# Kernel tuning notes

Measured on AMD Instinct MI355X. Metric: run time of the kernel, lower is better.

The kernel has to match this reference:

```python
import jax, jax.numpy as jnp
import numpy as np

E = 1024   # d_model
H = 16     # nhead
DH = E // H
F = 4096   # dim_feedforward
B, S = 4, 1024
EPS = 1e-5


def setup_inputs() -> dict:
    key = jax.random.key(0)
    ks = jax.random.split(key, 12)
    s = 0.02
    return {
        "src": jax.random.normal(ks[0], (B, S, E), jnp.float32),
        "src_mask": jnp.zeros((S, S), jnp.float32),
        "w_qkv": jax.random.normal(ks[1], (3 * E, E), jnp.float32) * s,
        "b_qkv": jnp.zeros((3 * E,), jnp.float32),
        "w_o": jax.random.normal(ks[2], (E, E), jnp.float32) * s,
        "b_o": jnp.zeros((E,), jnp.float32),
        "w1": jax.random.normal(ks[3], (F, E), jnp.float32) * s,
        "b1": jnp.zeros((F,), jnp.float32),
        "w2": jax.random.normal(ks[4], (E, F), jnp.float32) * s,
        "b2": jnp.zeros((E,), jnp.float32),
        "ln1_g": jnp.ones((E,), jnp.float32),
        "ln1_b": jnp.zeros((E,), jnp.float32),
        "ln2_g": jnp.ones((E,), jnp.float32),
        "ln2_b": jnp.zeros((E,), jnp.float32),
    }


def _layer_norm(x, g, b):
    mu = jnp.mean(x, axis=-1, keepdims=True)
    var = jnp.mean(jnp.square(x - mu), axis=-1, keepdims=True)
    return (x - mu) * jax.lax.rsqrt(var + EPS) * g + b


def reference(src, src_mask, w_qkv, b_qkv, w_o, b_o, w1, b1, w2, b2,
              ln1_g, ln1_b, ln2_g, ln2_b):
    # dropout in eval mode (identity). Math matches nn.MultiheadAttention
    # with need_weights=True, average_attn_weights=False.
    b, s, e = src.shape
    qkv = src @ w_qkv.T + b_qkv                      # [B,S,3E]
    q, k, v = jnp.split(qkv, 3, axis=-1)
    q = q.reshape(b, s, H, DH)
    k = k.reshape(b, s, H, DH)
    v = v.reshape(b, s, H, DH)
    scale = 1.0 / np.sqrt(DH)
    scores = jnp.einsum('bqhd,bkhd->bhqk', q, k) * scale + src_mask  # [B,H,S,S]
    attn_weights = jax.nn.softmax(scores, axis=-1)                   # [B,H,S,S]
    ctx = jnp.einsum('bhqk,bkhd->bqhd', attn_weights, v).reshape(b, s, e)
    attn_out = ctx @ w_o.T + b_o
    x = _layer_norm(src + attn_out, ln1_g, ln1_b)
    ffn = jax.nn.relu(x @ w1.T + b1) @ w2.T + b2
    x = _layer_norm(x + ffn, ln2_g, ln2_b)
    return x, attn_weights
```

## Files before the change

kernel.cpp:

```cpp
#include <hip/hip_runtime.h>
#include <cstdint>

typedef __bf16 bf16;
typedef bf16 bf16x8 __attribute__((ext_vector_type(8)));
typedef bf16 bf16x4 __attribute__((ext_vector_type(4)));
typedef float f32x4 __attribute__((ext_vector_type(4)));
typedef uint32_t u32;

static constexpr int E_ = 1024;
static constexpr int H_ = 16;
static constexpr int DH_ = 64;
static constexpr int F_ = 4096;
static constexpr int B_ = 4;
static constexpr int S_ = 1024;
static constexpr long TOK = (long)B_ * S_;

__device__ static __forceinline__ void gld16(const void* g, void* l) {
  __builtin_amdgcn_global_load_lds(
      (const __attribute__((address_space(1))) u32*)g,
      (__attribute__((address_space(3))) u32*)l, 16, 0, 0);
}

__device__ __forceinline__ f32x4 mfma16(bf16x8 a, bf16x8 b, f32x4 c) {
  return __builtin_amdgcn_mfma_f32_16x16x32_bf16(a, b, c, 0, 0, 0);
}

__global__ __launch_bounds__(256) void f2b_kernel(const float* __restrict__ in,
                                                  bf16* __restrict__ out, int n8) {
  int v = blockIdx.x * 256 + threadIdx.x;
  if (v >= n8) return;
  const float4* p = (const float4*)in + (long)v * 2;
  float4 a = p[0], b = p[1];
  bf16x8 o = {(bf16)a.x, (bf16)a.y, (bf16)a.z, (bf16)a.w,
              (bf16)b.x, (bf16)b.y, (bf16)b.z, (bf16)b.w};
  *((bf16x8*)out + v) = o;
}

enum { EPI_BIAS_F32 = 0, EPI_BIAS_RELU_BF16 = 1, EPI_QKV = 2, EPI_BIAS_RES_F32 = 3 };

template <int EPI>
__global__ __launch_bounds__(256, 2) void gemm_nt(
    const bf16* __restrict__ A, const bf16* __restrict__ Bm,
    float* __restrict__ Cf, bf16* __restrict__ Cb,
    bf16* __restrict__ Qh, bf16* __restrict__ Kh, bf16* __restrict__ Vt,
    const float* __restrict__ bias, const float* __restrict__ res,
    int K, int ldc) {
  __shared__ bf16 As[128 * 64];
  __shared__ bf16 Bs[128 * 64];
  const int tid = threadIdx.x, lane = tid & 63, wave = tid >> 6;
  const int quad = lane >> 4, l16 = lane & 15;
  const int wm = wave >> 1, wn = wave & 1;
  const int row0 = blockIdx.y * 128, col0 = blockIdx.x * 128;

  const long ldab = (long)K * 2;
  const char* Ag = (const char*)A +
                   (long)(row0 + wave * 32 + (lane >> 3)) * ldab + (lane & 7) * 16;
  const char* Bg = (const char*)Bm +
                   (long)(col0 + wave * 32 + (lane >> 3)) * ldab + (lane & 7) * 16;
  char* Al = (char*)As + wave * 4096 + lane * 16;
  char* Bl = (char*)Bs + wave * 4096 + lane * 16;

  f32x4 acc[4][4];
#pragma unroll
  for (int i = 0; i < 4; i++)
#pragma unroll
    for (int j = 0; j < 4; j++) acc[i][j] = (f32x4){0.f, 0.f, 0.f, 0.f};

  for (int k0 = 0; k0 < K; k0 += 64) {
    __syncthreads();
#pragma unroll
    for (int c = 0; c < 4; c++) gld16(Ag + (long)c * 8 * ldab + k0 * 2, Al + c * 1024);
#pragma unroll
    for (int c = 0; c < 4; c++) gld16(Bg + (long)c * 8 * ldab + k0 * 2, Bl + c * 1024);
    __syncthreads();
#pragma unroll
    for (int kk = 0; kk < 2; kk++) {
      bf16x8 af[4], bfr[4];
#pragma unroll
      for (int i = 0; i < 4; i++)
        af[i] = *(const bf16x8*)&As[(wm * 64 + i * 16 + l16) * 64 + kk * 32 + quad * 8];
#pragma unroll
      for (int j = 0; j < 4; j++)
        bfr[j] = *(const bf16x8*)&Bs[(wn * 64 + j * 16 + l16) * 64 + kk * 32 + quad * 8];
#pragma unroll
      for (int i = 0; i < 4; i++)
#pragma unroll
        for (int j = 0; j < 4; j++) acc[i][j] = mfma16(af[i], bfr[j], acc[i][j]);
    }
  }

#pragma unroll
  for (int i = 0; i < 4; i++)
#pragma unroll
    for (int j = 0; j < 4; j++)
#pragma unroll
      for (int r = 0; r < 4; r++) {
        int row = row0 + wm * 64 + i * 16 + quad * 4 + r;
        int col = col0 + wn * 64 + j * 16 + l16;
        float v = acc[i][j][r];
        if constexpr (EPI == EPI_BIAS_F32) {
          Cf[(long)row * ldc + col] = v + bias[col];
        } else if constexpr (EPI == EPI_BIAS_RES_F32) {
          Cf[(long)row * ldc + col] = v + bias[col] + res[(long)row * ldc + col];
        } else if constexpr (EPI == EPI_BIAS_RELU_BF16) {
          Cb[(long)row * ldc + col] = (bf16)fmaxf(v + bias[col], 0.f);
        } else {
          float t = v + bias[col];
          int b_ = row >> 10, s_ = row & 1023;
          int which = col >> 10, nn = col & 1023;
          int h_ = nn >> 6, d_ = nn & 63;
          if (which == 2) {
            Vt[(((long)(b_ * H_ + h_)) * DH_ + d_) * S_ + s_] = (bf16)t;
          } else {
            long q = (((long)(b_ * H_ + h_)) * S_ + s_) * DH_ + d_;
            if (which == 0) Qh[q] = (bf16)t;
            else Kh[q] = (bf16)t;
          }
        }
      }
}

__global__ __launch_bounds__(256, 2) void attn_pass1(
    const bf16* __restrict__ Q, const bf16* __restrict__ K,
    const float* __restrict__ mask, float* __restrict__ rowsum) {
  __shared__ bf16 Qs[128 * 64];
  __shared__ bf16 Ks[128 * 64];
  const int tid = threadIdx.x, lane = tid & 63, wave = tid >> 6;
  const int quad = lane >> 4, l16 = lane & 15;
  const int q0 = blockIdx.x * 128, bh = blockIdx.y;
  const bf16* Qb = Q + ((long)bh * S_ + q0) * DH_;
  const bf16* Kb = K + (long)bh * S_ * DH_;

  {
    const char* g = (const char*)Qb + wave * 4096 + lane * 16;
    char* l = (char*)Qs + wave * 4096 + lane * 16;
#pragma unroll
    for (int c = 0; c < 4; c++) gld16(g + c * 1024, l + c * 1024);
  }

  float rs[2][4];
#pragma unroll
  for (int i = 0; i < 2; i++)
#pragma unroll
    for (int r = 0; r < 4; r++) rs[i][r] = 0.f;

  for (int t = 0; t < 8; t++) {
    __syncthreads();
    {
      const char* g = (const char*)Kb + (long)t * 16384 + wave * 4096 + lane * 16;
      char* l = (char*)Ks + wave * 4096 + lane * 16;
#pragma unroll
      for (int c = 0; c < 4; c++) gld16(g + c * 1024, l + c * 1024);
    }
    __syncthreads();
    f32x4 acc[2][8];
#pragma unroll
    for (int i = 0; i < 2; i++)
#pragma unroll
      for (int j = 0; j < 8; j++) acc[i][j] = (f32x4){0.f, 0.f, 0.f, 0.f};
#pragma unroll
    for (int kk = 0; kk < 2; kk++) {
      bf16x8 af[2], bfr[8];
#pragma unroll
      for (int i = 0; i < 2; i++)
        af[i] = *(const bf16x8*)&Qs[(wave * 32 + i * 16 + l16) * 64 + kk * 32 + quad * 8];
#pragma unroll
      for (int j = 0; j < 8; j++)
        bfr[j] = *(const bf16x8*)&Ks[(j * 16 + l16) * 64 + kk * 32 + quad * 8];
#pragma unroll
      for (int i = 0; i < 2; i++)
#pragma unroll
        for (int j = 0; j < 8; j++) acc[i][j] = mfma16(af[i], bfr[j], acc[i][j]);
    }
#pragma unroll
    for (int i = 0; i < 2; i++)
#pragma unroll
      for (int j = 0; j < 8; j++)
#pragma unroll
        for (int r = 0; r < 4; r++) {
          int qr = q0 + wave * 32 + i * 16 + quad * 4 + r;
          int gcol = t * 128 + j * 16 + l16;
          float sv = acc[i][j][r] * 0.125f + mask[(long)qr * S_ + gcol];
          rs[i][r] += __expf(sv);
        }
  }
#pragma unroll
  for (int i = 0; i < 2; i++)
#pragma unroll
    for (int r = 0; r < 4; r++) {
      float v = rs[i][r];
      v += __shfl_xor(v, 1);
      v += __shfl_xor(v, 2);
      v += __shfl_xor(v, 4);
      v += __shfl_xor(v, 8);
      if (l16 == 0)
        rowsum[(long)bh * S_ + q0 + wave * 32 + i * 16 + quad * 4 + r] = v;
    }
}

__global__ __launch_bounds__(256, 2) void attn_pass2(
    const bf16* __restrict__ Q, const bf16* __restrict__ K,
    const bf16* __restrict__ V, const float* __restrict__ mask,
    const float* __restrict__ rowsum, float* __restrict__ W,
    bf16* __restrict__ ctxb) {
  __shared__ bf16 Qs[128 * 64];
  __shared__ bf16 Ks[128 * 64];
  __shared__ bf16 Ps[128 * 136];
  const int tid = threadIdx.x, lane = tid & 63, wave = tid >> 6;
  const int quad = lane >> 4, l16 = lane & 15;
  const int q0 = blockIdx.x * 128, bh = blockIdx.y;
  const bf16* Qb = Q + ((long)bh * S_ + q0) * DH_;
  const bf16* Kb = K + (long)bh * S_ * DH_;
  const bf16* Vb = V + (long)bh * DH_ * S_;

  float rinv[2][4];
#pragma unroll
  for (int i = 0; i < 2; i++)
#pragma unroll
    for (int r = 0; r < 4; r++)
      rinv[i][r] =
          1.0f / rowsum[(long)bh * S_ + q0 + wave * 32 + i * 16 + quad * 4 + r];

  {
    const char* g = (const char*)Qb + wave * 4096 + lane * 16;
    char* l = (char*)Qs + wave * 4096 + lane * 16;
#pragma unroll
    for (int c = 0; c < 4; c++) gld16(g + c * 1024, l + c * 1024);
  }

  f32x4 cacc[2][4];
#pragma unroll
  for (int i = 0; i < 2; i++)
#pragma unroll
    for (int j = 0; j < 4; j++) cacc[i][j] = (f32x4){0.f, 0.f, 0.f, 0.f};

  for (int t = 0; t < 8; t++) {
    __syncthreads();
    {
      const char* g = (const char*)Kb + (long)t * 16384 + wave * 4096 + lane * 16;
      char* l = (char*)Ks + wave * 4096 + lane * 16;
#pragma unroll
      for (int c = 0; c < 4; c++) gld16(g + c * 1024, l + c * 1024);
    }
    __syncthreads();
    f32x4 acc[2][8];
#pragma unroll
    for (int i = 0; i < 2; i++)
#pragma unroll
      for (int j = 0; j < 8; j++) acc[i][j] = (f32x4){0.f, 0.f, 0.f, 0.f};
#pragma unroll
    for (int kk = 0; kk < 2; kk++) {
      bf16x8 af[2], bfr[8];
#pragma unroll
      for (int i = 0; i < 2; i++)
        af[i] = *(const bf16x8*)&Qs[(wave * 32 + i * 16 + l16) * 64 + kk * 32 + quad * 8];
#pragma unroll
      for (int j = 0; j < 8; j++)
        bfr[j] = *(const bf16x8*)&Ks[(j * 16 + l16) * 64 + kk * 32 + quad * 8];
#pragma unroll
      for (int i = 0; i < 2; i++)
#pragma unroll
        for (int j = 0; j < 8; j++) acc[i][j] = mfma16(af[i], bfr[j], acc[i][j]);
    }
#pragma unroll
    for (int i = 0; i < 2; i++)
#pragma unroll
      for (int j = 0; j < 8; j++)
#pragma unroll
        for (int r = 0; r < 4; r++) {
          int ql = wave * 32 + i * 16 + quad * 4 + r;
          int qr = q0 + ql;
          int col = j * 16 + l16, gcol = t * 128 + col;
          float u = __expf(acc[i][j][r] * 0.125f + mask[(long)qr * S_ + gcol]) *
                    rinv[i][r];
          __builtin_nontemporal_store(u, &W[((long)bh * S_ + qr) * S_ + gcol]);
          Ps[ql * 136 + col] = (bf16)u;
        }
    __syncthreads();
#pragma unroll
    for (int kk = 0; kk < 4; kk++) {
      bf16x8 pf[2], vf[4];
#pragma unroll
      for (int i = 0; i < 2; i++)
        pf[i] = *(const bf16x8*)&Ps[(wave * 32 + i * 16 + l16) * 136 + kk * 32 + quad * 8];
#pragma unroll
      for (int j = 0; j < 4; j++)
        vf[j] = *(const bf16x8*)(Vb + (long)(j * 16 + l16) * S_ + t * 128 +
                                 kk * 32 + quad * 8);
#pragma unroll
      for (int i = 0; i < 2; i++)
#pragma unroll
        for (int j = 0; j < 4; j++) cacc[i][j] = mfma16(pf[i], vf[j], cacc[i][j]);
    }
  }
  const int b_ = bh >> 4, h_ = bh & 15;
#pragma unroll
  for (int i = 0; i < 2; i++)
#pragma unroll
    for (int j = 0; j < 4; j++)
#pragma unroll
      for (int r = 0; r < 4; r++) {
        int qr = q0 + wave * 32 + i * 16 + quad * 4 + r;
        ctxb[((long)b_ * S_ + qr) * E_ + h_ * 64 + j * 16 + l16] =
            (bf16)cacc[i][j][r];
      }
}

__global__ __launch_bounds__(256) void ln_kernel(
    const float* __restrict__ a, const float* __restrict__ g,
    const float* __restrict__ beta, float* __restrict__ outf,
    bf16* __restrict__ outb) {
  const int tid = threadIdx.x;
  const int wave = tid >> 6, lane = tid & 63;
  long base = (long)blockIdx.x * E_ + tid * 4;
  float4 x = *(const float4*)(a + base);
  float s = x.x + x.y + x.z + x.w;
  float sq = x.x * x.x + x.y * x.y + x.z * x.z + x.w * x.w;
#pragma unroll
  for (int o = 32; o; o >>= 1) { s += __shfl_xor(s, o); sq += __shfl_xor(sq, o); }
  __shared__ float rs[4], rq[4];
  if (!lane) { rs[wave] = s; rq[wave] = sq; }
  __syncthreads();
  s = rs[0] + rs[1] + rs[2] + rs[3];
  sq = rq[0] + rq[1] + rq[2] + rq[3];
  float mu = s * (1.f / E_);
  float var = sq * (1.f / E_) - mu * mu;
  float rstd = rsqrtf(var + 1e-5f);
  int c = tid * 4;
  float4 gg = *(const float4*)(g + c);
  float4 bb = *(const float4*)(beta + c);
  float o0 = (x.x - mu) * rstd * gg.x + bb.x;
  float o1 = (x.y - mu) * rstd * gg.y + bb.y;
  float o2 = (x.z - mu) * rstd * gg.z + bb.z;
  float o3 = (x.w - mu) * rstd * gg.w + bb.w;
  if (outf) *(float4*)(outf + base) = make_float4(o0, o1, o2, o3);
  if (outb) {
    bf16x4 ob = {(bf16)o0, (bf16)o1, (bf16)o2, (bf16)o3};
    *(bf16x4*)(outb + base) = ob;
  }
}

extern "C" void kernel_launch(void* const* d_in, const int* in_sizes, int n_in,
                              void* d_out, int out_size, void* d_ws, size_t ws_size,
                              hipStream_t stream) {
  const float* src   = (const float*)d_in[0];
  const float* mask  = (const float*)d_in[1];
  const float* w_qkv = (const float*)d_in[2];
  const float* b_qkv = (const float*)d_in[3];
  const float* w_o   = (const float*)d_in[4];
  const float* b_o   = (const float*)d_in[5];
  const float* w1    = (const float*)d_in[6];
  const float* b1    = (const float*)d_in[7];
  const float* w2    = (const float*)d_in[8];
  const float* b2    = (const float*)d_in[9];
  const float* ln1g  = (const float*)d_in[10];
  const float* ln1b  = (const float*)d_in[11];
  const float* ln2g  = (const float*)d_in[12];
  const float* ln2b  = (const float*)d_in[13];

  float* out = (float*)d_out;
  float* attnW = out + TOK * E_;

  char* w = (char*)d_ws;
  auto alloc = [&](size_t bytes) {
    void* p = w;
    w += (bytes + 255) & ~(size_t)255;
    return p;
  };
  bf16* srcb  = (bf16*)alloc(TOK * E_ * 2);
  bf16* wqkvb = (bf16*)alloc((size_t)3 * E_ * E_ * 2);
  bf16* wob   = (bf16*)alloc((size_t)E_ * E_ * 2);
  bf16* w1b   = (bf16*)alloc((size_t)F_ * E_ * 2);
  bf16* w2b   = (bf16*)alloc((size_t)E_ * F_ * 2);
  bf16* Qh    = (bf16*)alloc((size_t)B_ * H_ * S_ * DH_ * 2);
  bf16* Kh    = (bf16*)alloc((size_t)B_ * H_ * S_ * DH_ * 2);
  bf16* Vt    = (bf16*)alloc((size_t)B_ * H_ * DH_ * S_ * 2);
  bf16* ctxb  = (bf16*)alloc(TOK * E_ * 2);
  float* attn_out = (float*)alloc(TOK * E_ * 4);
  float* x1f  = (float*)alloc(TOK * E_ * 4);
  bf16* x1b   = (bf16*)alloc(TOK * E_ * 2);
  bf16* h1b   = (bf16*)alloc(TOK * (size_t)F_ * 2);
  float* ffn2 = (float*)alloc(TOK * E_ * 4);
  float* rowsum = (float*)alloc((size_t)B_ * H_ * S_ * 4);

  auto f2b = [&](const float* in, bf16* o, long n) {
    int n8 = (int)(n / 8);
    f2b_kernel<<<(n8 + 255) / 256, 256, 0, stream>>>(in, o, n8);
  };
  f2b(src, srcb, TOK * E_);
  f2b(w_qkv, wqkvb, (long)3 * E_ * E_);
  f2b(w_o, wob, (long)E_ * E_);
  f2b(w1, w1b, (long)F_ * E_);
  f2b(w2, w2b, (long)E_ * F_);

  gemm_nt<EPI_QKV><<<dim3(3 * E_ / 128, TOK / 128), 256, 0, stream>>>(
      srcb, wqkvb, nullptr, nullptr, Qh, Kh, Vt, b_qkv, nullptr, E_, 0);

  attn_pass1<<<dim3(S_ / 128, B_ * H_), 256, 0, stream>>>(Qh, Kh, mask, rowsum);
  attn_pass2<<<dim3(S_ / 128, B_ * H_), 256, 0, stream>>>(Qh, Kh, Vt, mask,
                                                          rowsum, attnW, ctxb);

  gemm_nt<EPI_BIAS_RES_F32><<<dim3(E_ / 128, TOK / 128), 256, 0, stream>>>(
      ctxb, wob, attn_out, nullptr, nullptr, nullptr, nullptr, b_o, src, E_, E_);

  ln_kernel<<<TOK, 256, 0, stream>>>(attn_out, ln1g, ln1b, x1f, x1b);

  gemm_nt<EPI_BIAS_RELU_BF16><<<dim3(F_ / 128, TOK / 128), 256, 0, stream>>>(
      x1b, w1b, nullptr, h1b, nullptr, nullptr, nullptr, b1, nullptr, E_, F_);

  gemm_nt<EPI_BIAS_RES_F32><<<dim3(E_ / 128, TOK / 128), 256, 0, stream>>>(
      h1b, w2b, ffn2, nullptr, nullptr, nullptr, nullptr, b2, x1f, F_, E_);

  ln_kernel<<<TOK, 256, 0, stream>>>(ffn2, ln2g, ln2b, out, nullptr);
}
```

Before: 648.5 us.

## Merge fp32-to-bf16 casts, add BN-templated GEMM, transpose V through LDS

Five separate fp32-to-bf16 conversion launches become one kernel that dispatches on flat index ranges. The GEMM gets a BN template parameter, and the two N=1024 GEMMs use 64-wide tiles so more blocks fill the GPU. The QKV epilogue now stages V tiles through a swizzled LDS transpose so it can write V^T with 16-byte vector stores instead of strided scalar stores. The smaller tiles lower per-block data reuse and add more blocks, and the merged cast kernel hardcodes the buffer offsets.

```diff
diff --git a/kernel.cpp b/kernel.cpp
--- a/kernel.cpp
+++ b/kernel.cpp
@@ -25,99 +25,148 @@
   return __builtin_amdgcn_mfma_f32_16x16x32_bf16(a, b, c, 0, 0, 0);
 }
 
-__global__ __launch_bounds__(256) void f2b_kernel(const float* __restrict__ in,
-                                                  bf16* __restrict__ out, int n8) {
-  int v = blockIdx.x * 256 + threadIdx.x;
-  if (v >= n8) return;
-  const float4* p = (const float4*)in + (long)v * 2;
+__global__ __launch_bounds__(256) void f2b_all(
+    const float* __restrict__ s0, bf16* __restrict__ d0,
+    const float* __restrict__ s1, bf16* __restrict__ d1,
+    const float* __restrict__ s2, bf16* __restrict__ d2,
+    const float* __restrict__ s3, bf16* __restrict__ d3,
+    const float* __restrict__ s4, bf16* __restrict__ d4) {
+  long v = (long)blockIdx.x * 256 + threadIdx.x;
+  const float* in;
+  bf16* out;
+  long off;
+  if (v < 524288)        { in = s0; out = d0; off = v; }
+  else if (v < 917504)   { in = s1; out = d1; off = v - 524288; }
+  else if (v < 1048576)  { in = s2; out = d2; off = v - 917504; }
+  else if (v < 1572864)  { in = s3; out = d3; off = v - 1048576; }
+  else                   { in = s4; out = d4; off = v - 1572864; }
+  const float4* p = (const float4*)in + off * 2;
   float4 a = p[0], b = p[1];
   bf16x8 o = {(bf16)a.x, (bf16)a.y, (bf16)a.z, (bf16)a.w,
               (bf16)b.x, (bf16)b.y, (bf16)b.z, (bf16)b.w};
-  *((bf16x8*)out + v) = o;
+  *((bf16x8*)out + off) = o;
 }
 
 enum { EPI_BIAS_F32 = 0, EPI_BIAS_RELU_BF16 = 1, EPI_QKV = 2, EPI_BIAS_RES_F32 = 3 };
 
-template <int EPI>
+template <int EPI, int BN>
 __global__ __launch_bounds__(256, 2) void gemm_nt(
     const bf16* __restrict__ A, const bf16* __restrict__ Bm,
     float* __restrict__ Cf, bf16* __restrict__ Cb,
     bf16* __restrict__ Qh, bf16* __restrict__ Kh, bf16* __restrict__ Vt,
     const float* __restrict__ bias, const float* __restrict__ res,
     int K, int ldc) {
-  __shared__ bf16 As[128 * 64];
-  __shared__ bf16 Bs[128 * 64];
+  constexpr int NJ = BN / 32;
+  __shared__ bf16 Sm[128 * 64 + BN * 64];
+  bf16* As = Sm;
+  bf16* Bs = Sm + 128 * 64;
   const int tid = threadIdx.x, lane = tid & 63, wave = tid >> 6;
   const int quad = lane >> 4, l16 = lane & 15;
   const int wm = wave >> 1, wn = wave & 1;
-  const int row0 = blockIdx.y * 128, col0 = blockIdx.x * 128;
+  const int row0 = blockIdx.y * 128, col0 = blockIdx.x * BN;
 
   const long ldab = (long)K * 2;
   const char* Ag = (const char*)A +
                    (long)(row0 + wave * 32 + (lane >> 3)) * ldab + (lane & 7) * 16;
   const char* Bg = (const char*)Bm +
-                   (long)(col0 + wave * 32 + (lane >> 3)) * ldab + (lane & 7) * 16;
-  char* Al = (char*)As + wave * 4096 + lane * 16;
-  char* Bl = (char*)Bs + wave * 4096 + lane * 16;
-
-  f32x4 acc[4][4];
+                   (long)(col0 + wave * (BN / 4) + (lane >> 3)) * ldab + (lane & 7) * 16;
+  char* Al = (char*)As + (wave * 32 + (lane >> 3)) * 128 + (lane & 7) * 16;
+  char* Bl = (char*)Bs + (wave * (BN / 4) + (lane >> 3)) * 128 + (lane & 7) * 16;
+
+  f32x4 acc[4][NJ];
 #pragma unroll
   for (int i = 0; i < 4; i++)
 #pragma unroll
-    for (int j = 0; j < 4; j++) acc[i][j] = (f32x4){0.f, 0.f, 0.f, 0.f};
+    for (int j = 0; j < NJ; j++) acc[i][j] = (f32x4){0.f, 0.f, 0.f, 0.f};
 
   for (int k0 = 0; k0 < K; k0 += 64) {
     __syncthreads();
 #pragma unroll
     for (int c = 0; c < 4; c++) gld16(Ag + (long)c * 8 * ldab + k0 * 2, Al + c * 1024);
 #pragma unroll
-    for (int c = 0; c < 4; c++) gld16(Bg + (long)c * 8 * ldab + k0 * 2, Bl + c * 1024);
+    for (int c = 0; c < BN / 32; c++) gld16(Bg + (long)c * 8 * ldab + k0 * 2, Bl + c * 1024);
     __syncthreads();
 #pragma unroll
     for (int kk = 0; kk < 2; kk++) {
-      bf16x8 af[4], bfr[4];
+      bf16x8 af[4], bfr[NJ];
 #pragma unroll
       for (int i = 0; i < 4; i++)
         af[i] = *(const bf16x8*)&As[(wm * 64 + i * 16 + l16) * 64 + kk * 32 + quad * 8];
 #pragma unroll
-      for (int j = 0; j < 4; j++)
-        bfr[j] = *(const bf16x8*)&Bs[(wn * 64 + j * 16 + l16) * 64 + kk * 32 + quad * 8];
+      for (int j = 0; j < NJ; j++)
+        bfr[j] = *(const bf16x8*)&Bs[(wn * (BN / 2) + j * 16 + l16) * 64 + kk * 32 + quad * 8];
 #pragma unroll
       for (int i = 0; i < 4; i++)
 #pragma unroll
-        for (int j = 0; j < 4; j++) acc[i][j] = mfma16(af[i], bfr[j], acc[i][j]);
-    }
-  }
-
-#pragma unroll
-  for (int i = 0; i < 4; i++)
-#pragma unroll
-    for (int j = 0; j < 4; j++)
-#pragma unroll
-      for (int r = 0; r < 4; r++) {
-        int row = row0 + wm * 64 + i * 16 + quad * 4 + r;
-        int col = col0 + wn * 64 + j * 16 + l16;
-        float v = acc[i][j][r];
-        if constexpr (EPI == EPI_BIAS_F32) {
-          Cf[(long)row * ldc + col] = v + bias[col];
-        } else if constexpr (EPI == EPI_BIAS_RES_F32) {
-          Cf[(long)row * ldc + col] = v + bias[col] + res[(long)row * ldc + col];
-        } else if constexpr (EPI == EPI_BIAS_RELU_BF16) {
-          Cb[(long)row * ldc + col] = (bf16)fmaxf(v + bias[col], 0.f);
-        } else {
-          float t = v + bias[col];
-          int b_ = row >> 10, s_ = row & 1023;
-          int which = col >> 10, nn = col & 1023;
-          int h_ = nn >> 6, d_ = nn & 63;
-          if (which == 2) {
-            Vt[(((long)(b_ * H_ + h_)) * DH_ + d_) * S_ + s_] = (bf16)t;
-          } else {
+        for (int j = 0; j < NJ; j++) acc[i][j] = mfma16(af[i], bfr[j], acc[i][j]);
+    }
+  }
+
+  if constexpr (EPI == EPI_QKV) {
+    const int which = col0 >> 10;
+    if (which == 2) {
+      bf16* T = Sm;
+      __syncthreads();
+#pragma unroll
+      for (int i = 0; i < 4; i++)
+#pragma unroll
+        for (int j = 0; j < NJ; j++)
+#pragma unroll
+          for (int r = 0; r < 4; r++) {
+            int row_l = wm * 64 + i * 16 + quad * 4 + r;
+            int col_l = wn * 64 + j * 16 + l16;
+            float t = acc[i][j][r] + bias[col0 + col_l];
+            T[col_l * 128 + (row_l ^ ((col_l & 7) << 4))] = (bf16)t;
+          }
+      __syncthreads();
+      const int b_ = row0 >> 10;
+      const int s0 = row0 & 1023;
+#pragma unroll
+      for (int g = 0; g < 8; g++) {
+        int col_l = wave * 32 + g * 4 + quad;
+        int nn = (col0 + col_l) & 1023;
+        int h_ = nn >> 6, d_ = nn & 63;
+        int sl = l16 * 8;
+        bf16x8 vv = *(const bf16x8*)&T[col_l * 128 + (sl ^ ((col_l & 7) << 4))];
+        *(bf16x8*)&Vt[(((long)(b_ * H_ + h_)) * DH_ + d_) * S_ + s0 + sl] = vv;
+      }
+    } else {
+#pragma unroll
+      for (int i = 0; i < 4; i++)
+#pragma unroll
+        for (int j = 0; j < NJ; j++)
+#pragma unroll
+          for (int r = 0; r < 4; r++) {
+            int row = row0 + wm * 64 + i * 16 + quad * 4 + r;
+            int col = col0 + wn * (BN / 2) + j * 16 + l16;
+            float t = acc[i][j][r] + bias[col];
+            int b_ = row >> 10, s_ = row & 1023;
+            int nn = col & 1023;
+            int h_ = nn >> 6, d_ = nn & 63;
             long q = (((long)(b_ * H_ + h_)) * S_ + s_) * DH_ + d_;
             if (which == 0) Qh[q] = (bf16)t;
             else Kh[q] = (bf16)t;
           }
+    }
+  } else {
+#pragma unroll
+    for (int i = 0; i < 4; i++)
+#pragma unroll
+      for (int j = 0; j < NJ; j++)
+#pragma unroll
+        for (int r = 0; r < 4; r++) {
+          int row = row0 + wm * 64 + i * 16 + quad * 4 + r;
+          int col = col0 + wn * (BN / 2) + j * 16 + l16;
+          float v = acc[i][j][r];
+          if constexpr (EPI == EPI_BIAS_F32) {
+            Cf[(long)row * ldc + col] = v + bias[col];
+          } else if constexpr (EPI == EPI_BIAS_RES_F32) {
+            Cf[(long)row * ldc + col] = v + bias[col] + res[(long)row * ldc + col];
+          } else {
+            Cb[(long)row * ldc + col] = (bf16)fmaxf(v + bias[col], 0.f);
+          }
         }
-      }
+  }
 }
 
 __global__ __launch_bounds__(256, 2) void attn_pass1(
@@ -383,32 +432,25 @@
   float* ffn2 = (float*)alloc(TOK * E_ * 4);
   float* rowsum = (float*)alloc((size_t)B_ * H_ * S_ * 4);
 
-  auto f2b = [&](const float* in, bf16* o, long n) {
-    int n8 = (int)(n / 8);
-    f2b_kernel<<<(n8 + 255) / 256, 256, 0, stream>>>(in, o, n8);
-  };
-  f2b(src, srcb, TOK * E_);
-  f2b(w_qkv, wqkvb, (long)3 * E_ * E_);
-  f2b(w_o, wob, (long)E_ * E_);
-  f2b(w1, w1b, (long)F_ * E_);
-  f2b(w2, w2b, (long)E_ * F_);
-
-  gemm_nt<EPI_QKV><<<dim3(3 * E_ / 128, TOK / 128), 256, 0, stream>>>(
+  f2b_all<<<8192, 256, 0, stream>>>(src, srcb, w_qkv, wqkvb, w_o, wob,
+                                    w1, w1b, w2, w2b);
+
+  gemm_nt<EPI_QKV, 128><<<dim3(3 * E_ / 128, TOK / 128), 256, 0, stream>>>(
       srcb, wqkvb, nullptr, nullptr, Qh, Kh, Vt, b_qkv, nullptr, E_, 0);
 
   attn_pass1<<<dim3(S_ / 128, B_ * H_), 256, 0, stream>>>(Qh, Kh, mask, rowsum);
   attn_pass2<<<dim3(S_ / 128, B_ * H_), 256, 0, stream>>>(Qh, Kh, Vt, mask,
                                                           rowsum, attnW, ctxb);
 
-  gemm_nt<EPI_BIAS_RES_F32><<<dim3(E_ / 128, TOK / 128), 256, 0, stream>>>(
+  gemm_nt<EPI_BIAS_RES_F32, 64><<<dim3(E_ / 64, TOK / 128), 256, 0, stream>>>(
       ctxb, wob, attn_out, nullptr, nullptr, nullptr, nullptr, b_o, src, E_, E_);
 
   ln_kernel<<<TOK, 256, 0, stream>>>(attn_out, ln1g, ln1b, x1f, x1b);
 
-  gemm_nt<EPI_BIAS_RELU_BF16><<<dim3(F_ / 128, TOK / 128), 256, 0, stream>>>(
+  gemm_nt<EPI_BIAS_RELU_BF16, 128><<<dim3(F_ / 128, TOK / 128), 256, 0, stream>>>(
       x1b, w1b, nullptr, h1b, nullptr, nullptr, nullptr, b1, nullptr, E_, F_);
 
-  gemm_nt<EPI_BIAS_RES_F32><<<dim3(E_ / 128, TOK / 128), 256, 0, stream>>>(
+  gemm_nt<EPI_BIAS_RES_F32, 64><<<dim3(E_ / 64, TOK / 128), 256, 0, stream>>>(
       h1b, w2b, ffn2, nullptr, nullptr, nullptr, nullptr, b2, x1f, F_, E_);
 
   ln_kernel<<<TOK, 256, 0, stream>>>(ffn2, ln2g, ln2b, out, nullptr);
```

Measured after the change: 614.0 us. -5.3%, faster.
